# Kernel tuning notes

Measured on AMD Instinct MI355X. Metric: run time of the kernel, lower is better.

## Reference

```python
import jax, jax.numpy as jnp
import numpy as np

T, B, D, A, L = 256, 256, 512, 32, 3
EPS = 1e-6

def _layernorm(x, scale, bias):
    mu = jnp.mean(x, axis=-1, keepdims=True)
    var = jnp.mean(jnp.square(x - mu), axis=-1, keepdims=True)
    return (x - mu) * jax.lax.rsqrt(var + EPS) * scale + bias

def setup_inputs() -> dict:
    key = jax.random.key(0)
    ks = jax.random.split(key, 16)
    def orth(k, shape, scale):
        a = jax.random.normal(k, shape, dtype=jnp.float32)
        q, r = jnp.linalg.qr(a)
        q = q * jnp.sign(jnp.diagonal(r))
        return (scale * q).astype(jnp.float32)
    inp = {
        'hidden': jnp.zeros((B, D), jnp.float32),
        'obs': jax.random.normal(ks[0], (T, B, D), jnp.float32),
        'dones': jax.random.randint(ks[1], (T, B), 0, 2) > 0,
        'avail_actions': jax.random.randint(ks[2], (T, B, A), 0, 2).astype(jnp.int32),
        # MLP stack: 3 Dense(D) + LayerNorm
        'Wm': jnp.stack([orth(jax.random.fold_in(ks[3], l), (D, D), np.sqrt(2)) for l in range(L)]),
        'bm': jnp.zeros((L, D), jnp.float32),
        'lns': jnp.ones((L, D), jnp.float32),
        'lnb': jnp.zeros((L, D), jnp.float32),
        # GRUCell params: input denses ir/iz/in (with bias), hidden denses hr/hz (no bias), hn (bias)
        'Wi': jnp.stack([jax.random.normal(jax.random.fold_in(ks[4], g), (D, D), jnp.float32) / np.sqrt(D) for g in range(3)]),
        'bi': jnp.zeros((3, D), jnp.float32),
        'Wh': jnp.stack([orth(jax.random.fold_in(ks[5], g), (D, D), 1.0) for g in range(3)]),
        'bhn': jnp.zeros((D,), jnp.float32),
        # actor head
        'Wo': orth(ks[6], (D, D), 2.0),
        'bo': jnp.zeros((D,), jnp.float32),
        'ln2s': jnp.ones((D,), jnp.float32),
        'ln2b': jnp.zeros((D,), jnp.float32),
        'Wa': orth(ks[7], (D, A), 0.01),
        'ba': jnp.zeros((A,), jnp.float32),
    }
    return inp

def reference(hidden, obs, dones, avail_actions, Wm, bm, lns, lnb, Wi, bi, Wh, bhn, Wo, bo, ln2s, ln2b, Wa, ba):
    # MLP encoder: Dense -> LayerNorm -> ReLU, x num_layers
    e = obs  # [T,B,D]
    for l in range(Wm.shape[0]):
        e = jax.nn.relu(_layernorm(e @ Wm[l] + bm[l], lns[l], lnb[l]))
    # time-scanned GRU with reset-masked carry (reset -> zeros carry)
    def step(h, xs):
        x, d = xs  # x:[B,D], d:[B]
        h = jnp.where(d[:, None], jnp.zeros_like(h), h)
        r = jax.nn.sigmoid(x @ Wi[0] + bi[0] + h @ Wh[0])
        z = jax.nn.sigmoid(x @ Wi[1] + bi[1] + h @ Wh[1])
        n = jnp.tanh(x @ Wi[2] + bi[2] + r * (h @ Wh[2] + bhn))
        h_new = (1.0 - z) * n + z * h
        return h_new, h_new
    hidden, y = jax.lax.scan(step, hidden, (e, dones))  # y:[T,B,D]
    # actor head
    am = jax.nn.relu(_layernorm(y @ Wo + bo, ln2s, ln2b))
    logits = am @ Wa + ba
    unavail = 1.0 - avail_actions.astype(logits.dtype)
    action_logits = logits - unavail * 1e10
    return hidden, action_logits
```

## Files before the change

### kernel.cpp

```cpp
#include <hip/hip_runtime.h>
#include <hip/hip_bf16.h>
#include <math.h>


#define TTT 256
#define BBB 256
#define DDD 512
#define ACT 32
#define MMM (TTT*BBB)

typedef short bf16x8 __attribute__((ext_vector_type(8)));
typedef float f32x4 __attribute__((ext_vector_type(4)));
typedef unsigned short u16;

__device__ inline u16 f2bf(float f) {
    unsigned int u = __float_as_uint(f);
    u += 0x7fffu + ((u >> 16) & 1u);
    return (u16)(u >> 16);
}
__device__ inline float bf2f(u16 h) { return __uint_as_float(((unsigned int)h) << 16); }

__global__ __launch_bounds__(256) void transpose_cvt_k(
    const float* __restrict__ in, u16* __restrict__ out, int ostride)
{
    __shared__ float tile[32][33];
    const int c = threadIdx.x & 31;
    const int r0 = threadIdx.x >> 5;
    const int bx = blockIdx.x, by = blockIdx.y;
#pragma unroll
    for (int p = 0; p < 4; p++) {
        int r = r0 + p * 8;
        tile[r][c] = in[(size_t)(by * 32 + r) * DDD + bx * 32 + c];
    }
    __syncthreads();
#pragma unroll
    for (int p = 0; p < 4; p++) {
        int r = r0 + p * 8;
        out[(size_t)(bx * 32 + r) * ostride + by * 32 + c] = f2bf(tile[c][r]);
    }
}

template<bool AF32>
__global__ __launch_bounds__(256) void gemm_bf16_k(
    const void* __restrict__ Aptr, const u16* __restrict__ Bt,
    const float* __restrict__ bias, u16* __restrict__ C, int N)
{
    __shared__ u16 As[128 * 64];
    __shared__ u16 Bs[128 * 64];
    const int tid = threadIdx.x;
    const int row0 = blockIdx.x * 128;
    const int col0 = blockIdx.y * 128;
    const int lane = tid & 63, wid = tid >> 6;
    const int wr = wid >> 1, wc = wid & 1;
    const int lm = lane & 15, lq = lane >> 4;

    f32x4 acc[4][4];
#pragma unroll
    for (int i = 0; i < 4; i++)
#pragma unroll
        for (int j = 0; j < 4; j++) acc[i][j] = (f32x4){0.f, 0.f, 0.f, 0.f};

    for (int kc = 0; kc < 8; kc++) {
        const int k0 = kc * 64;
#pragma unroll
        for (int p = 0; p < 4; p++) {
            int g = p * 256 + tid;
            int row = g >> 3, j = g & 7;
            bf16x8 v;
            if (AF32) {
                const float* s = (const float*)Aptr + (size_t)(row0 + row) * DDD + k0 + j * 8;
                float4 a0 = *(const float4*)s;
                float4 a1 = *(const float4*)(s + 4);
                v[0] = (short)f2bf(a0.x); v[1] = (short)f2bf(a0.y);
                v[2] = (short)f2bf(a0.z); v[3] = (short)f2bf(a0.w);
                v[4] = (short)f2bf(a1.x); v[5] = (short)f2bf(a1.y);
                v[6] = (short)f2bf(a1.z); v[7] = (short)f2bf(a1.w);
            } else {
                v = *(const bf16x8*)((const u16*)Aptr + (size_t)(row0 + row) * DDD + k0 + j * 8);
            }
            *(bf16x8*)(As + row * 64 + ((j ^ (row & 7)) << 3)) = v;
        }
#pragma unroll
        for (int p = 0; p < 4; p++) {
            int g = p * 256 + tid;
            int n = g >> 3, j = g & 7;
            bf16x8 v = *(const bf16x8*)(Bt + (size_t)(col0 + n) * DDD + k0 + j * 8);
            *(bf16x8*)(Bs + n * 64 + ((j ^ (n & 7)) << 3)) = v;
        }
        __syncthreads();
#pragma unroll
        for (int ks = 0; ks < 2; ks++) {
            bf16x8 af[4], bfr[4];
#pragma unroll
            for (int i = 0; i < 4; i++) {
                int row = wr * 64 + i * 16 + lm;
                af[i] = *(const bf16x8*)(As + row * 64 + (((ks * 4 + lq) ^ (row & 7)) << 3));
            }
#pragma unroll
            for (int j = 0; j < 4; j++) {
                int n = wc * 64 + j * 16 + lm;
                bfr[j] = *(const bf16x8*)(Bs + n * 64 + (((ks * 4 + lq) ^ (n & 7)) << 3));
            }
#pragma unroll
            for (int i = 0; i < 4; i++)
#pragma unroll
                for (int j = 0; j < 4; j++)
                    acc[i][j] = __builtin_amdgcn_mfma_f32_16x16x32_bf16(af[i], bfr[j], acc[i][j], 0, 0, 0);
        }
        __syncthreads();
    }
#pragma unroll
    for (int j = 0; j < 4; j++) {
        int col = col0 + wc * 64 + j * 16 + lm;
        float bj = bias[col];
#pragma unroll
        for (int i = 0; i < 4; i++) {
            int rb = row0 + wr * 64 + i * 16 + lq * 4;
#pragma unroll
            for (int r = 0; r < 4; r++)
                C[(size_t)(rb + r) * N + col] = f2bf(acc[i][j][r] + bj);
        }
    }
}

__global__ __launch_bounds__(256) void ln_relu_k(
    u16* __restrict__ X, const float* __restrict__ gamma, const float* __restrict__ beta)
{
    const int tid = threadIdx.x;
    const int lane = tid & 63;
    const size_t row = (size_t)blockIdx.x * 4 + (tid >> 6);
    const int c0 = lane * 8;
    u16* px = X + row * DDD + c0;
    bf16x8 v = *(const bf16x8*)px;
    float f[8]; float s = 0.f, s2 = 0.f;
#pragma unroll
    for (int i = 0; i < 8; i++) { f[i] = bf2f((u16)v[i]); s += f[i]; s2 += f[i] * f[i]; }
#pragma unroll
    for (int off = 32; off; off >>= 1) { s += __shfl_xor(s, off); s2 += __shfl_xor(s2, off); }
    float mu = s * (1.f / (float)DDD);
    float rs = rsqrtf(s2 * (1.f / (float)DDD) - mu * mu + 1e-6f);
    float4 g0 = *(const float4*)(gamma + c0), g1 = *(const float4*)(gamma + c0 + 4);
    float4 b0 = *(const float4*)(beta + c0),  b1 = *(const float4*)(beta + c0 + 4);
    float gg[8] = {g0.x, g0.y, g0.z, g0.w, g1.x, g1.y, g1.z, g1.w};
    float bb[8] = {b0.x, b0.y, b0.z, b0.w, b1.x, b1.y, b1.z, b1.w};
    bf16x8 o;
#pragma unroll
    for (int i = 0; i < 8; i++) {
        float yv = (f[i] - mu) * rs * gg[i] + bb[i];
        o[i] = (short)f2bf(fmaxf(yv, 0.f));
    }
    *(bf16x8*)px = o;
}

__global__ __launch_bounds__(256) void logits_k(
    const u16* __restrict__ AM, const float* __restrict__ Wa,
    const float* __restrict__ ba, const int* __restrict__ avail,
    float* __restrict__ out)
{
    __shared__ float xs[8][DDD];
    const int tid = threadIdx.x;
    const size_t row0 = (size_t)blockIdx.x * 8;
    for (int g = tid; g < 8 * 64; g += 256) {
        int r = g >> 6, c8 = (g & 63) * 8;
        bf16x8 v = *(const bf16x8*)(AM + (row0 + r) * DDD + c8);
#pragma unroll
        for (int i = 0; i < 8; i++) xs[r][c8 + i] = bf2f((u16)v[i]);
    }
    __syncthreads();
    const int r = tid >> 5, a = tid & 31;
    float acc = 0.f;
    for (int k = 0; k < DDD; k += 4) {
        float4 xv = *(const float4*)&xs[r][k];
        acc = fmaf(xv.x, Wa[(k + 0) * ACT + a], acc);
        acc = fmaf(xv.y, Wa[(k + 1) * ACT + a], acc);
        acc = fmaf(xv.z, Wa[(k + 2) * ACT + a], acc);
        acc = fmaf(xv.w, Wa[(k + 3) * ACT + a], acc);
    }
    size_t o = (row0 + r) * ACT + a;
    float v = acc + ba[a];
    if (avail[o] == 0) v -= 1e10f;
    out[o] = v;
}

__global__ __launch_bounds__(256) void depth_build_k(
    const int* __restrict__ dones,
    int* __restrict__ keyA, int* __restrict__ pidxA,
    int* __restrict__ counts, int* __restrict__ maxk)
{
    __shared__ int lc[512];
    __shared__ int lmax;
    const int b = threadIdx.x;
    lc[b] = 0; lc[b + 256] = 0;
    if (b == 0) lmax = 0;
    __syncthreads();
    int dprev = 0, mx = 0;
    for (int t = 0; t < TTT; t++) {
        int pos = t * BBB + b;
        int d, pi, k;
        if (dones[pos] != 0)       { d = 0; pi = -1;       k = 0; }
        else if (t == 0)           { d = 0; pi = -2 - b;   k = 1; }
        else                       { d = dprev + 1; pi = pos - BBB; k = d + 1; }
        keyA[pos] = k; pidxA[pos] = pi;
        atomicAdd(&lc[k], 1);
        mx = max(mx, k);
        dprev = d;
    }
    atomicMax(&lmax, mx);
    __syncthreads();
    counts[b] = lc[b];
    counts[b + 256] = lc[b + 256];
    if (b == 0) *maxk = lmax;
}

__global__ void scan_k(const int* __restrict__ counts, int* __restrict__ offs)
{
    if (threadIdx.x == 0) {
        int s = 0;
        for (int i = 0; i < 512; i++) { offs[i] = s; s += counts[i]; }
    }
}

__global__ __launch_bounds__(256) void scatter_k(
    const int* __restrict__ keyA, const int* __restrict__ offs,
    int* __restrict__ cursor, int* __restrict__ list)
{
    __shared__ int lcnt[512];
    __shared__ int lbase[512];
    const int tid = threadIdx.x;
    lcnt[tid] = 0; lcnt[tid + 256] = 0;
    __syncthreads();
    int pos = blockIdx.x * 256 + tid;
    int k = keyA[pos];
    int rank = atomicAdd(&lcnt[k], 1);
    __syncthreads();
    for (int q = tid; q < 512; q += 256) {
        int c = lcnt[q];
        lbase[q] = c ? atomicAdd(&cursor[q], c) : 0;
    }
    __syncthreads();
    list[offs[k] + lbase[k] + rank] = pos;
}

__device__ inline void grid_barrier(int* cnt, int* gen, int nblk)
{
    __syncthreads();
    if (threadIdx.x == 0) {
        __threadfence();
        int g = __hip_atomic_load(gen, __ATOMIC_RELAXED, __HIP_MEMORY_SCOPE_AGENT);
        int a = __hip_atomic_fetch_add(cnt, 1, __ATOMIC_ACQ_REL, __HIP_MEMORY_SCOPE_AGENT);
        if (a == nblk - 1) {
            __hip_atomic_store(cnt, 0, __ATOMIC_RELAXED, __HIP_MEMORY_SCOPE_AGENT);
            __hip_atomic_store(gen, g + 1, __ATOMIC_RELEASE, __HIP_MEMORY_SCOPE_AGENT);
        } else {
            while (__hip_atomic_load(gen, __ATOMIC_RELAXED, __HIP_MEMORY_SCOPE_AGENT) == g)
                __builtin_amdgcn_s_sleep(4);
            (void)__hip_atomic_load(gen, __ATOMIC_ACQUIRE, __HIP_MEMORY_SCOPE_AGENT);
        }
        __threadfence();
    }
    __syncthreads();
}

template<bool YF32>
__global__ __launch_bounds__(256, 2) void gru_depth_k(
    const u16* __restrict__ E, const float* __restrict__ hidden,
    const u16* __restrict__ Wstk, const float* __restrict__ bi,
    const float* __restrict__ bhn,
    const int* __restrict__ list, const int* __restrict__ offs,
    const int* __restrict__ counts, const int* __restrict__ maxk,
    const int* __restrict__ pidxA,
    void* __restrict__ Yv, float* __restrict__ hid_out,
    int* __restrict__ barCnt, int* __restrict__ barGen)
{
    __shared__ u16 As[64 * 256];
    __shared__ int posL[64], pidxL[64];
    __shared__ int sAnyH;
    const int tid = threadIdx.x;
    const int w = tid >> 6, lane = tid & 63;
    const int lm = lane & 15, lq = lane >> 4;
    const int nblk = gridDim.x;
    const int e   = blockIdx.x & 7;
    const int xb  = blockIdx.x >> 3;
    const int nxb = nblk >> 3;

    const int MK = *maxk;
    for (int k = 0; k <= MK; k++) {
        const int nd = counts[k];
        const int off = offs[k];
        const int ntiles = (nd + 63) >> 6;
        const int ntl = (ntiles - e + 7) >> 3;
        const int njl = (ntl > 0) ? (ntl << 2) : 0;
        for (int lj = xb; lj < njl; lj += nxb) {
            const int rt = ((lj >> 2) << 3) + e;
            const int panel = lj & 3;
            bool hasH = false;
            if (tid < 64) {
                int idx = rt * 64 + tid;
                int p = (idx < nd) ? list[off + idx] : -1;
                int pi = (p >= 0) ? pidxA[p] : -1;
                posL[tid] = p;
                pidxL[tid] = pi;
                hasH = (p >= 0) && (pi != -1);
                unsigned long long m = __ballot(hasH);
                if (tid == 0) sAnyH = (m != 0ULL);
            }
            __syncthreads();
            const bool skipH = !sAnyH;

            f32x4 a01[4][4], aX[4][2], aH[4][2];
#pragma unroll
            for (int mt = 0; mt < 4; mt++) {
#pragma unroll
                for (int q = 0; q < 4; q++) a01[mt][q] = (f32x4){0.f, 0.f, 0.f, 0.f};
#pragma unroll
                for (int q = 0; q < 2; q++) {
                    aX[mt][q] = (f32x4){0.f, 0.f, 0.f, 0.f};
                    aH[mt][q] = (f32x4){0.f, 0.f, 0.f, 0.f};
                }
            }

            const int cb = panel * 128 + w * 32;
            const u16* wp[6];
#pragma unroll
            for (int ct = 0; ct < 6; ct++) {
                int gate = ct >> 1;
                int nglob = gate * 512 + cb + ((ct & 1) << 4) + lm;
                wp[ct] = Wstk + (size_t)nglob * 1024 + lq * 8;
            }

            const int nkc = skipH ? 2 : 4;
            for (int kc = 0; kc < nkc; kc++) {
#pragma unroll
                for (int it = 0; it < 8; it++) {
                    int g = it * 256 + tid;
                    int row = g >> 5, jg = g & 31;
                    int kglob = kc * 256 + jg * 8;
                    bf16x8 v = (bf16x8){0, 0, 0, 0, 0, 0, 0, 0};
                    int p = posL[row];
                    if (p >= 0) {
                        if (kglob < 512) {
                            v = *(const bf16x8*)(E + (size_t)p * DDD + kglob);
                        } else {
                            int k2 = kglob - 512;
                            int pi = pidxL[row];
                            if (pi >= 0) {
                                if (YF32) {
                                    const float* s = (const float*)Yv + (size_t)pi * DDD + k2;
                                    float4 a0 = *(const float4*)s;
                                    float4 a1 = *(const float4*)(s + 4);
                                    v[0] = (short)f2bf(a0.x); v[1] = (short)f2bf(a0.y);
                                    v[2] = (short)f2bf(a0.z); v[3] = (short)f2bf(a0.w);
                                    v[4] = (short)f2bf(a1.x); v[5] = (short)f2bf(a1.y);
                                    v[6] = (short)f2bf(a1.z); v[7] = (short)f2bf(a1.w);
                                } else {
                                    v = *(const bf16x8*)((const u16*)Yv + (size_t)pi * DDD + k2);
                                }
                            } else if (pi <= -2) {
                                const float* s = hidden + (size_t)(-pi - 2) * DDD + k2;
                                float4 a0 = *(const float4*)s;
                                float4 a1 = *(const float4*)(s + 4);
                                v[0] = (short)f2bf(a0.x); v[1] = (short)f2bf(a0.y);
                                v[2] = (short)f2bf(a0.z); v[3] = (short)f2bf(a0.w);
                                v[4] = (short)f2bf(a1.x); v[5] = (short)f2bf(a1.y);
                                v[6] = (short)f2bf(a1.z); v[7] = (short)f2bf(a1.w);
                            }
                        }
                    }
                    *(bf16x8*)(As + row * 256 + ((jg ^ (row & 31)) << 3)) = v;
                }
                __syncthreads();

                const bool xpart = (kc < 2);
                const int kgb = kc * 256;
                bf16x8 bfA[6], bfB[6];

#define LOADW(B, KG) \
    _Pragma("unroll") \
    for (int ct = 0; ct < 6; ct++) B[ct] = *(const bf16x8*)(wp[ct] + (KG));

#define COMPW(B, S) \
    _Pragma("unroll") \
    for (int mt = 0; mt < 4; mt++) { \
        int row = mt * 16 + lm; \
        int jgr = (S) * 4 + lq; \
        bf16x8 af = *(const bf16x8*)(As + row * 256 + ((jgr ^ (row & 31)) << 3)); \
        a01[mt][0] = __builtin_amdgcn_mfma_f32_16x16x32_bf16(af, B[0], a01[mt][0], 0, 0, 0); \
        a01[mt][1] = __builtin_amdgcn_mfma_f32_16x16x32_bf16(af, B[1], a01[mt][1], 0, 0, 0); \
        a01[mt][2] = __builtin_amdgcn_mfma_f32_16x16x32_bf16(af, B[2], a01[mt][2], 0, 0, 0); \
        a01[mt][3] = __builtin_amdgcn_mfma_f32_16x16x32_bf16(af, B[3], a01[mt][3], 0, 0, 0); \
        if (xpart) { \
            aX[mt][0] = __builtin_amdgcn_mfma_f32_16x16x32_bf16(af, B[4], aX[mt][0], 0, 0, 0); \
            aX[mt][1] = __builtin_amdgcn_mfma_f32_16x16x32_bf16(af, B[5], aX[mt][1], 0, 0, 0); \
        } else { \
            aH[mt][0] = __builtin_amdgcn_mfma_f32_16x16x32_bf16(af, B[4], aH[mt][0], 0, 0, 0); \
            aH[mt][1] = __builtin_amdgcn_mfma_f32_16x16x32_bf16(af, B[5], aH[mt][1], 0, 0, 0); \
        } \
    }

                LOADW(bfA, kgb + 0 * 32);
#pragma unroll
                for (int sp = 0; sp < 4; sp++) {
                    const int s0 = sp * 2, s1 = sp * 2 + 1;
                    LOADW(bfB, kgb + s1 * 32);
                    COMPW(bfA, s0);
                    if (sp < 3) { LOADW(bfA, kgb + (s1 + 1) * 32); }
                    COMPW(bfB, s1);
                }
#undef LOADW
#undef COMPW
                __syncthreads();
            }

#pragma unroll
            for (int mt = 0; mt < 4; mt++) {
#pragma unroll
                for (int r = 0; r < 4; r++) {
                    int row = mt * 16 + lq * 4 + r;
                    int p = posL[row];
                    if (p < 0) continue;
                    int pi = pidxL[row];
#pragma unroll
                    for (int ct = 0; ct < 2; ct++) {
                        int cglob = cb + ct * 16 + lm;
                        float rpre = a01[mt][ct][r]     + bi[cglob];
                        float zpre = a01[mt][2 + ct][r] + bi[512 + cglob];
                        float xn   = aX[mt][ct][r]      + bi[1024 + cglob];
                        float hn   = aH[mt][ct][r]      + bhn[cglob];
                        float rg = 1.f / (1.f + __expf(-rpre));
                        float zg = 1.f / (1.f + __expf(-zpre));
                        float targ = xn + rg * hn;
                        float t2 = __expf(-2.f * fabsf(targ));
                        float ng = copysignf((1.f - t2) / (1.f + t2), targ);
                        float hp = 0.f;
                        if (pi >= 0)
                            hp = YF32 ? ((const float*)Yv)[(size_t)pi * DDD + cglob]
                                      : bf2f(((const u16*)Yv)[(size_t)pi * DDD + cglob]);
                        else if (pi <= -2)
                            hp = hidden[(size_t)(-pi - 2) * DDD + cglob];
                        float hnew = (1.f - zg) * ng + zg * hp;
                        if (YF32) ((float*)Yv)[(size_t)p * DDD + cglob] = hnew;
                        else      ((u16*)Yv)[(size_t)p * DDD + cglob] = f2bf(hnew);
                    }
                }
            }
            __syncthreads();
        }
        grid_barrier(barCnt, barGen, nblk);
    }

    for (int i = blockIdx.x * 256 + tid; i < BBB * DDD; i += nblk * 256) {
        int b = i >> 9, c = i & 511;
        size_t yi = (size_t)(65280 + b) * DDD + c;
        hid_out[i] = YF32 ? ((const float*)Yv)[yi] : bf2f(((const u16*)Yv)[yi]);
    }
}

extern "C" void kernel_launch(void* const* d_in, const int* in_sizes, int n_in,
                              void* d_out, int out_size, void* d_ws, size_t ws_size,
                              hipStream_t stream)
{
    const float* hidden = (const float*)d_in[0];
    const float* obs    = (const float*)d_in[1];
    const int*   dones  = (const int*)d_in[2];
    const int*   avail  = (const int*)d_in[3];
    const float* Wm     = (const float*)d_in[4];
    const float* bm     = (const float*)d_in[5];
    const float* lns    = (const float*)d_in[6];
    const float* lnb    = (const float*)d_in[7];
    const float* Wi     = (const float*)d_in[8];
    const float* bi     = (const float*)d_in[9];
    const float* Wh     = (const float*)d_in[10];
    const float* bhn    = (const float*)d_in[11];
    const float* Wo     = (const float*)d_in[12];
    const float* bo     = (const float*)d_in[13];
    const float* ln2s   = (const float*)d_in[14];
    const float* ln2b   = (const float*)d_in[15];
    const float* Wa     = (const float*)d_in[16];
    const float* ba     = (const float*)d_in[17];
    float* out = (float*)d_out;

    char* w = (char*)d_ws;
    u16* Wstk = (u16*)w;  w += (size_t)1536 * 1024 * 2;
    u16* WmT  = (u16*)w;  w += (size_t)3 * DDD * DDD * 2;
    u16* WoT  = (u16*)w;  w += (size_t)DDD * DDD * 2;
    int* meta = (int*)w;  w += 8192;
    int* counts = meta;
    int* offs   = meta + 512;
    int* cursor = meta + 1024;
    int* maxk   = meta + 1536;
    int* barCnt = meta + 1568;
    int* barGen = meta + 1600;
    int* keyA   = (int*)w;  w += (size_t)MMM * 4;
    int* pidxA  = (int*)w;  w += (size_t)MMM * 4;
    int* list   = (int*)w;  w += (size_t)MMM * 4;
    u16* P = (u16*)w;       w += (size_t)MMM * DDD * 2;
    void* Yv = (void*)w;
    const size_t base = (size_t)(w - (char*)d_ws);
    const bool yf32 = (ws_size >= base + (size_t)MMM * DDD * 4);

    dim3 tgrid(16, 16);
    for (int l = 0; l < 3; l++)
        transpose_cvt_k<<<tgrid, 256, 0, stream>>>(Wm + (size_t)l * DDD * DDD, WmT + (size_t)l * DDD * DDD, DDD);
    transpose_cvt_k<<<tgrid, 256, 0, stream>>>(Wo, WoT, DDD);
    for (int g = 0; g < 3; g++) {
        transpose_cvt_k<<<tgrid, 256, 0, stream>>>(Wi + (size_t)g * DDD * DDD, Wstk + (size_t)g * 512 * 1024, 1024);
        transpose_cvt_k<<<tgrid, 256, 0, stream>>>(Wh + (size_t)g * DDD * DDD, Wstk + (size_t)g * 512 * 1024 + 512, 1024);
    }
    hipMemsetAsync(meta, 0, 8192, stream);

    depth_build_k<<<1, 256, 0, stream>>>(dones, keyA, pidxA, counts, maxk);
    scan_k<<<1, 64, 0, stream>>>(counts, offs);
    scatter_k<<<MMM / 256, 256, 0, stream>>>(keyA, offs, cursor, list);

    u16* Yq = (u16*)Yv;
    gemm_bf16_k<true><<<dim3(MMM / 128, 4), 256, 0, stream>>>(obs, WmT, bm, P, DDD);
    ln_relu_k<<<dim3(MMM / 4), 256, 0, stream>>>(P, lns, lnb);
    gemm_bf16_k<false><<<dim3(MMM / 128, 4), 256, 0, stream>>>(P, WmT + (size_t)DDD * DDD, bm + DDD, Yq, DDD);
    ln_relu_k<<<dim3(MMM / 4), 256, 0, stream>>>(Yq, lns + DDD, lnb + DDD);
    gemm_bf16_k<false><<<dim3(MMM / 128, 4), 256, 0, stream>>>(Yq, WmT + (size_t)2 * DDD * DDD, bm + 2 * DDD, P, DDD);
    ln_relu_k<<<dim3(MMM / 4), 256, 0, stream>>>(P, lns + 2 * DDD, lnb + 2 * DDD);

    {
        const void* fptr = yf32 ? (const void*)gru_depth_k<true>
                                : (const void*)gru_depth_k<false>;
        int occ = 0;
        hipError_t e = hipOccupancyMaxActiveBlocksPerMultiprocessor(&occ, fptr, 256, 0);
        if (e != hipSuccess || occ < 1) occ = 2;
        if (occ > 4) occ = 4;
        dim3 grid(occ * 256);
        if (yf32)
            gru_depth_k<true><<<grid, 256, 0, stream>>>(
                P, hidden, Wstk, bi, bhn, list, offs, counts, maxk, pidxA,
                Yv, out, barCnt, barGen);
        else
            gru_depth_k<false><<<grid, 256, 0, stream>>>(
                P, hidden, Wstk, bi, bhn, list, offs, counts, maxk, pidxA,
                Yv, out, barCnt, barGen);
    }

    if (yf32)
        gemm_bf16_k<true><<<dim3(MMM / 128, 4), 256, 0, stream>>>(Yv, WoT, bo, P, DDD);
    else
        gemm_bf16_k<false><<<dim3(MMM / 128, 4), 256, 0, stream>>>(Yv, WoT, bo, P, DDD);
    ln_relu_k<<<dim3(MMM / 4), 256, 0, stream>>>(P, ln2s, ln2b);
    logits_k<<<dim3(MMM / 8), 256, 0, stream>>>(P, Wa, ba, avail, out + BBB * DDD);
}
```

Measured before the change: 2.181 ms.

## Partition GRU depth scheduling per XCD and replace grid barrier with per-XCD counters

Splits the batch into 8 groups of 32 sequences, one per XCD (blockIdx & 7), building separate depth histograms, offsets and work lists for each group. Each group of blocks then advances through its own depth levels and synchronises only with blocks on the same XCD through a monotonic per-group counter, instead of a global generation barrier across all blocks. This removes cross-XCD barrier traffic and lets groups with shallower reset depth finish early. The cost is possible load imbalance between groups, and correctness relies on the blocks sharing an index modulo 8 seeing each other's writes at agent scope.

```diff
diff --git a/kernel.cpp b/kernel.cpp
--- a/kernel.cpp
+++ b/kernel.cpp
@@ -19,6 +19,8 @@
     return (u16)(u >> 16);
 }
 __device__ inline float bf2f(u16 h) { return __uint_as_float(((unsigned int)h) << 16); }
+
+#define AL_RLX(p)  __hip_atomic_load((p), __ATOMIC_RELAXED, __HIP_MEMORY_SCOPE_AGENT)
 
 __global__ __launch_bounds__(256) void transpose_cvt_k(
     const float* __restrict__ in, u16* __restrict__ out, int ostride)
@@ -187,11 +189,12 @@
     int* __restrict__ keyA, int* __restrict__ pidxA,
     int* __restrict__ counts, int* __restrict__ maxk)
 {
-    __shared__ int lc[512];
-    __shared__ int lmax;
+    __shared__ int lc[8 * 512];
+    __shared__ int lmax[8];
     const int b = threadIdx.x;
-    lc[b] = 0; lc[b + 256] = 0;
-    if (b == 0) lmax = 0;
+    const int e = b >> 5;
+    for (int i = b; i < 8 * 512; i += 256) lc[i] = 0;
+    if (b < 8) lmax[b] = 0;
     __syncthreads();
     int dprev = 0, mx = 0;
     for (int t = 0; t < TTT; t++) {
@@ -201,22 +204,22 @@
         else if (t == 0)           { d = 0; pi = -2 - b;   k = 1; }
         else                       { d = dprev + 1; pi = pos - BBB; k = d + 1; }
         keyA[pos] = k; pidxA[pos] = pi;
-        atomicAdd(&lc[k], 1);
+        atomicAdd(&lc[e * 512 + k], 1);
         mx = max(mx, k);
         dprev = d;
     }
-    atomicMax(&lmax, mx);
-    __syncthreads();
-    counts[b] = lc[b];
-    counts[b + 256] = lc[b + 256];
-    if (b == 0) *maxk = lmax;
+    atomicMax(&lmax[e], mx);
+    __syncthreads();
+    for (int i = b; i < 8 * 512; i += 256) counts[i] = lc[i];
+    if (b < 8) maxk[b] = lmax[b];
 }
 
 __global__ void scan_k(const int* __restrict__ counts, int* __restrict__ offs)
 {
-    if (threadIdx.x == 0) {
+    int e = threadIdx.x;
+    if (e < 8) {
         int s = 0;
-        for (int i = 0; i < 512; i++) { offs[i] = s; s += counts[i]; }
+        for (int i = 0; i < 512; i++) { offs[e * 512 + i] = s; s += counts[e * 512 + i]; }
     }
 }
 
@@ -224,155 +227,119 @@
     const int* __restrict__ keyA, const int* __restrict__ offs,
     int* __restrict__ cursor, int* __restrict__ list)
 {
-    __shared__ int lcnt[512];
-    __shared__ int lbase[512];
+    __shared__ int lcnt[8 * 512];
+    __shared__ int lbase[8 * 512];
     const int tid = threadIdx.x;
-    lcnt[tid] = 0; lcnt[tid + 256] = 0;
+    for (int i = tid; i < 8 * 512; i += 256) lcnt[i] = 0;
     __syncthreads();
     int pos = blockIdx.x * 256 + tid;
+    int b = pos & 255;
+    int e = b >> 5;
     int k = keyA[pos];
-    int rank = atomicAdd(&lcnt[k], 1);
-    __syncthreads();
-    for (int q = tid; q < 512; q += 256) {
+    int rank = atomicAdd(&lcnt[e * 512 + k], 1);
+    __syncthreads();
+    for (int q = tid; q < 8 * 512; q += 256) {
         int c = lcnt[q];
         lbase[q] = c ? atomicAdd(&cursor[q], c) : 0;
     }
     __syncthreads();
-    list[offs[k] + lbase[k] + rank] = pos;
-}
-
-__device__ inline void grid_barrier(int* cnt, int* gen, int nblk)
-{
-    __syncthreads();
-    if (threadIdx.x == 0) {
-        __threadfence();
-        int g = __hip_atomic_load(gen, __ATOMIC_RELAXED, __HIP_MEMORY_SCOPE_AGENT);
-        int a = __hip_atomic_fetch_add(cnt, 1, __ATOMIC_ACQ_REL, __HIP_MEMORY_SCOPE_AGENT);
-        if (a == nblk - 1) {
-            __hip_atomic_store(cnt, 0, __ATOMIC_RELAXED, __HIP_MEMORY_SCOPE_AGENT);
-            __hip_atomic_store(gen, g + 1, __ATOMIC_RELEASE, __HIP_MEMORY_SCOPE_AGENT);
-        } else {
-            while (__hip_atomic_load(gen, __ATOMIC_RELAXED, __HIP_MEMORY_SCOPE_AGENT) == g)
-                __builtin_amdgcn_s_sleep(4);
-            (void)__hip_atomic_load(gen, __ATOMIC_ACQUIRE, __HIP_MEMORY_SCOPE_AGENT);
-        }
-        __threadfence();
-    }
-    __syncthreads();
+    list[e * 8192 + offs[e * 512 + k] + lbase[e * 512 + k] + rank] = pos;
 }
 
 template<bool YF32>
-__global__ __launch_bounds__(256, 2) void gru_depth_k(
+__device__ __forceinline__ void gru_job(
     const u16* __restrict__ E, const float* __restrict__ hidden,
     const u16* __restrict__ Wstk, const float* __restrict__ bi,
     const float* __restrict__ bhn,
-    const int* __restrict__ list, const int* __restrict__ offs,
-    const int* __restrict__ counts, const int* __restrict__ maxk,
-    const int* __restrict__ pidxA,
-    void* __restrict__ Yv, float* __restrict__ hid_out,
-    int* __restrict__ barCnt, int* __restrict__ barGen)
-{
-    __shared__ u16 As[64 * 256];
-    __shared__ int posL[64], pidxL[64];
-    __shared__ int sAnyH;
+    const int* __restrict__ list, const int* __restrict__ pidxA,
+    void* __restrict__ Yv,
+    int off, int nd, int rt, int panel,
+    u16* As, int* posL, int* pidxL, int* sAnyH)
+{
     const int tid = threadIdx.x;
     const int w = tid >> 6, lane = tid & 63;
     const int lm = lane & 15, lq = lane >> 4;
-    const int nblk = gridDim.x;
-    const int e   = blockIdx.x & 7;
-    const int xb  = blockIdx.x >> 3;
-    const int nxb = nblk >> 3;
-
-    const int MK = *maxk;
-    for (int k = 0; k <= MK; k++) {
-        const int nd = counts[k];
-        const int off = offs[k];
-        const int ntiles = (nd + 63) >> 6;
-        const int ntl = (ntiles - e + 7) >> 3;
-        const int njl = (ntl > 0) ? (ntl << 2) : 0;
-        for (int lj = xb; lj < njl; lj += nxb) {
-            const int rt = ((lj >> 2) << 3) + e;
-            const int panel = lj & 3;
-            bool hasH = false;
-            if (tid < 64) {
-                int idx = rt * 64 + tid;
-                int p = (idx < nd) ? list[off + idx] : -1;
-                int pi = (p >= 0) ? pidxA[p] : -1;
-                posL[tid] = p;
-                pidxL[tid] = pi;
-                hasH = (p >= 0) && (pi != -1);
-                unsigned long long m = __ballot(hasH);
-                if (tid == 0) sAnyH = (m != 0ULL);
-            }
-            __syncthreads();
-            const bool skipH = !sAnyH;
-
-            f32x4 a01[4][4], aX[4][2], aH[4][2];
-#pragma unroll
-            for (int mt = 0; mt < 4; mt++) {
-#pragma unroll
-                for (int q = 0; q < 4; q++) a01[mt][q] = (f32x4){0.f, 0.f, 0.f, 0.f};
-#pragma unroll
-                for (int q = 0; q < 2; q++) {
-                    aX[mt][q] = (f32x4){0.f, 0.f, 0.f, 0.f};
-                    aH[mt][q] = (f32x4){0.f, 0.f, 0.f, 0.f};
+
+    bool hasH = false;
+    if (tid < 64) {
+        int idx = rt * 64 + tid;
+        int p = (idx < nd) ? list[off + idx] : -1;
+        int pi = (p >= 0) ? pidxA[p] : -1;
+        posL[tid] = p;
+        pidxL[tid] = pi;
+        hasH = (p >= 0) && (pi != -1);
+        unsigned long long m = __ballot(hasH);
+        if (tid == 0) *sAnyH = (m != 0ULL);
+    }
+    __syncthreads();
+    const bool skipH = !(*sAnyH);
+
+    f32x4 a01[4][4], aX[4][2], aH[4][2];
+#pragma unroll
+    for (int mt = 0; mt < 4; mt++) {
+#pragma unroll
+        for (int q = 0; q < 4; q++) a01[mt][q] = (f32x4){0.f, 0.f, 0.f, 0.f};
+#pragma unroll
+        for (int q = 0; q < 2; q++) {
+            aX[mt][q] = (f32x4){0.f, 0.f, 0.f, 0.f};
+            aH[mt][q] = (f32x4){0.f, 0.f, 0.f, 0.f};
+        }
+    }
+
+    const int cb = panel * 128 + w * 32;
+    const u16* wp[6];
+#pragma unroll
+    for (int ct = 0; ct < 6; ct++) {
+        int gate = ct >> 1;
+        int nglob = gate * 512 + cb + ((ct & 1) << 4) + lm;
+        wp[ct] = Wstk + (size_t)nglob * 1024 + lq * 8;
+    }
+
+    const int nkc = skipH ? 2 : 4;
+    for (int kc = 0; kc < nkc; kc++) {
+#pragma unroll
+        for (int it = 0; it < 8; it++) {
+            int g = it * 256 + tid;
+            int row = g >> 5, jg = g & 31;
+            int kglob = kc * 256 + jg * 8;
+            bf16x8 v = (bf16x8){0, 0, 0, 0, 0, 0, 0, 0};
+            int p = posL[row];
+            if (p >= 0) {
+                if (kglob < 512) {
+                    v = *(const bf16x8*)(E + (size_t)p * DDD + kglob);
+                } else {
+                    int k2 = kglob - 512;
+                    int pi = pidxL[row];
+                    if (pi >= 0) {
+                        if (YF32) {
+                            const float* s = (const float*)Yv + (size_t)pi * DDD + k2;
+                            float4 a0 = *(const float4*)s;
+                            float4 a1 = *(const float4*)(s + 4);
+                            v[0] = (short)f2bf(a0.x); v[1] = (short)f2bf(a0.y);
+                            v[2] = (short)f2bf(a0.z); v[3] = (short)f2bf(a0.w);
+                            v[4] = (short)f2bf(a1.x); v[5] = (short)f2bf(a1.y);
+                            v[6] = (short)f2bf(a1.z); v[7] = (short)f2bf(a1.w);
+                        } else {
+                            v = *(const bf16x8*)((const u16*)Yv + (size_t)pi * DDD + k2);
+                        }
+                    } else if (pi <= -2) {
+                        const float* s = hidden + (size_t)(-pi - 2) * DDD + k2;
+                        float4 a0 = *(const float4*)s;
+                        float4 a1 = *(const float4*)(s + 4);
+                        v[0] = (short)f2bf(a0.x); v[1] = (short)f2bf(a0.y);
+                        v[2] = (short)f2bf(a0.z); v[3] = (short)f2bf(a0.w);
+                        v[4] = (short)f2bf(a1.x); v[5] = (short)f2bf(a1.y);
+                        v[6] = (short)f2bf(a1.z); v[7] = (short)f2bf(a1.w);
+                    }
                 }
             }
-
-            const int cb = panel * 128 + w * 32;
-            const u16* wp[6];
-#pragma unroll
-            for (int ct = 0; ct < 6; ct++) {
-                int gate = ct >> 1;
-                int nglob = gate * 512 + cb + ((ct & 1) << 4) + lm;
-                wp[ct] = Wstk + (size_t)nglob * 1024 + lq * 8;
-            }
-
-            const int nkc = skipH ? 2 : 4;
-            for (int kc = 0; kc < nkc; kc++) {
-#pragma unroll
-                for (int it = 0; it < 8; it++) {
-                    int g = it * 256 + tid;
-                    int row = g >> 5, jg = g & 31;
-                    int kglob = kc * 256 + jg * 8;
-                    bf16x8 v = (bf16x8){0, 0, 0, 0, 0, 0, 0, 0};
-                    int p = posL[row];
-                    if (p >= 0) {
-                        if (kglob < 512) {
-                            v = *(const bf16x8*)(E + (size_t)p * DDD + kglob);
-                        } else {
-                            int k2 = kglob - 512;
-                            int pi = pidxL[row];
-                            if (pi >= 0) {
-                                if (YF32) {
-                                    const float* s = (const float*)Yv + (size_t)pi * DDD + k2;
-                                    float4 a0 = *(const float4*)s;
-                                    float4 a1 = *(const float4*)(s + 4);
-                                    v[0] = (short)f2bf(a0.x); v[1] = (short)f2bf(a0.y);
-                                    v[2] = (short)f2bf(a0.z); v[3] = (short)f2bf(a0.w);
-                                    v[4] = (short)f2bf(a1.x); v[5] = (short)f2bf(a1.y);
-                                    v[6] = (short)f2bf(a1.z); v[7] = (short)f2bf(a1.w);
-                                } else {
-                                    v = *(const bf16x8*)((const u16*)Yv + (size_t)pi * DDD + k2);
-                                }
-                            } else if (pi <= -2) {
-                                const float* s = hidden + (size_t)(-pi - 2) * DDD + k2;
-                                float4 a0 = *(const float4*)s;
-                                float4 a1 = *(const float4*)(s + 4);
-                                v[0] = (short)f2bf(a0.x); v[1] = (short)f2bf(a0.y);
-                                v[2] = (short)f2bf(a0.z); v[3] = (short)f2bf(a0.w);
-                                v[4] = (short)f2bf(a1.x); v[5] = (short)f2bf(a1.y);
-                                v[6] = (short)f2bf(a1.z); v[7] = (short)f2bf(a1.w);
-                            }
-                        }
-                    }
-                    *(bf16x8*)(As + row * 256 + ((jg ^ (row & 31)) << 3)) = v;
-                }
-                __syncthreads();
-
-                const bool xpart = (kc < 2);
-                const int kgb = kc * 256;
-                bf16x8 bfA[6], bfB[6];
+            *(bf16x8*)(As + row * 256 + ((jg ^ (row & 31)) << 3)) = v;
+        }
+        __syncthreads();
+
+        const bool xpart = (kc < 2);
+        const int kgb = kc * 256;
+        bf16x8 bfA[6], bfB[6];
 
 #define LOADW(B, KG) \
     _Pragma("unroll") \
@@ -397,61 +364,105 @@
         } \
     }
 
-                LOADW(bfA, kgb + 0 * 32);
-#pragma unroll
-                for (int sp = 0; sp < 4; sp++) {
-                    const int s0 = sp * 2, s1 = sp * 2 + 1;
-                    LOADW(bfB, kgb + s1 * 32);
-                    COMPW(bfA, s0);
-                    if (sp < 3) { LOADW(bfA, kgb + (s1 + 1) * 32); }
-                    COMPW(bfB, s1);
-                }
+        LOADW(bfA, kgb + 0 * 32);
+#pragma unroll
+        for (int sp = 0; sp < 4; sp++) {
+            const int s0 = sp * 2, s1 = sp * 2 + 1;
+            LOADW(bfB, kgb + s1 * 32);
+            COMPW(bfA, s0);
+            if (sp < 3) { LOADW(bfA, kgb + (s1 + 1) * 32); }
+            COMPW(bfB, s1);
+        }
 #undef LOADW
 #undef COMPW
-                __syncthreads();
+        __syncthreads();
+    }
+
+#pragma unroll
+    for (int mt = 0; mt < 4; mt++) {
+#pragma unroll
+        for (int r = 0; r < 4; r++) {
+            int row = mt * 16 + lq * 4 + r;
+            int p = posL[row];
+            if (p < 0) continue;
+            int pi = pidxL[row];
+#pragma unroll
+            for (int ct = 0; ct < 2; ct++) {
+                int cglob = cb + ct * 16 + lm;
+                float rpre = a01[mt][ct][r]     + bi[cglob];
+                float zpre = a01[mt][2 + ct][r] + bi[512 + cglob];
+                float xn   = aX[mt][ct][r]      + bi[1024 + cglob];
+                float hn   = aH[mt][ct][r]      + bhn[cglob];
+                float rg = 1.f / (1.f + __expf(-rpre));
+                float zg = 1.f / (1.f + __expf(-zpre));
+                float targ = xn + rg * hn;
+                float t2 = __expf(-2.f * fabsf(targ));
+                float ng = copysignf((1.f - t2) / (1.f + t2), targ);
+                float hp = 0.f;
+                if (pi >= 0)
+                    hp = YF32 ? ((const float*)Yv)[(size_t)pi * DDD + cglob]
+                              : bf2f(((const u16*)Yv)[(size_t)pi * DDD + cglob]);
+                else if (pi <= -2)
+                    hp = hidden[(size_t)(-pi - 2) * DDD + cglob];
+                float hnew = (1.f - zg) * ng + zg * hp;
+                if (YF32) ((float*)Yv)[(size_t)p * DDD + cglob] = hnew;
+                else      ((u16*)Yv)[(size_t)p * DDD + cglob] = f2bf(hnew);
             }
-
-#pragma unroll
-            for (int mt = 0; mt < 4; mt++) {
-#pragma unroll
-                for (int r = 0; r < 4; r++) {
-                    int row = mt * 16 + lq * 4 + r;
-                    int p = posL[row];
-                    if (p < 0) continue;
-                    int pi = pidxL[row];
-#pragma unroll
-                    for (int ct = 0; ct < 2; ct++) {
-                        int cglob = cb + ct * 16 + lm;
-                        float rpre = a01[mt][ct][r]     + bi[cglob];
-                        float zpre = a01[mt][2 + ct][r] + bi[512 + cglob];
-                        float xn   = aX[mt][ct][r]      + bi[1024 + cglob];
-                        float hn   = aH[mt][ct][r]      + bhn[cglob];
-                        float rg = 1.f / (1.f + __expf(-rpre));
-                        float zg = 1.f / (1.f + __expf(-zpre));
-                        float targ = xn + rg * hn;
-                        float t2 = __expf(-2.f * fabsf(targ));
-                        float ng = copysignf((1.f - t2) / (1.f + t2), targ);
-                        float hp = 0.f;
-                        if (pi >= 0)
-                            hp = YF32 ? ((const float*)Yv)[(size_t)pi * DDD + cglob]
-                                      : bf2f(((const u16*)Yv)[(size_t)pi * DDD + cglob]);
-                        else if (pi <= -2)
-                            hp = hidden[(size_t)(-pi - 2) * DDD + cglob];
-                        float hnew = (1.f - zg) * ng + zg * hp;
-                        if (YF32) ((float*)Yv)[(size_t)p * DDD + cglob] = hnew;
-                        else      ((u16*)Yv)[(size_t)p * DDD + cglob] = f2bf(hnew);
-                    }
-                }
-            }
-            __syncthreads();
-        }
-        grid_barrier(barCnt, barGen, nblk);
-    }
-
-    for (int i = blockIdx.x * 256 + tid; i < BBB * DDD; i += nblk * 256) {
-        int b = i >> 9, c = i & 511;
+        }
+    }
+    __syncthreads();
+}
+
+template<bool YF32>
+__global__ __launch_bounds__(256, 2) void gru_depth_k(
+    const u16* __restrict__ E, const float* __restrict__ hidden,
+    const u16* __restrict__ Wstk, const float* __restrict__ bi,
+    const float* __restrict__ bhn,
+    const int* __restrict__ list, const int* __restrict__ offs,
+    const int* __restrict__ counts, const int* __restrict__ maxk,
+    const int* __restrict__ pidxA,
+    void* __restrict__ Yv, float* __restrict__ hid_out,
+    int* __restrict__ xcdCnt)
+{
+    __shared__ u16 As[64 * 256];
+    __shared__ int posL[64], pidxL[64];
+    __shared__ int sAnyH;
+    const int tid = threadIdx.x;
+    const int nblk = gridDim.x;
+    const int e   = blockIdx.x & 7;
+    const int xb  = blockIdx.x >> 3;
+    const int nxb = nblk >> 3;
+
+    const int MKe = maxk[e];
+    const int* cnt_e = counts + e * 512;
+    const int* off_e = offs + e * 512;
+    const int lb = e * 8192;
+    int* cnt = xcdCnt + e * 32;
+    int round = 0;
+
+    for (int k = 0; k <= MKe; k++) {
+        const int nd = cnt_e[k];
+        const int off = lb + off_e[k];
+        const int njobs = ((nd + 63) >> 6) << 2;
+        for (int lj = xb; lj < njobs; lj += nxb) {
+            gru_job<YF32>(E, hidden, Wstk, bi, bhn, list, pidxA, Yv,
+                          off, nd, lj >> 2, lj & 3, As, posL, pidxL, &sAnyH);
+        }
+        ++round;
+        __syncthreads();
+        if (tid == 0) {
+            __hip_atomic_fetch_add(cnt, 1, __ATOMIC_RELAXED, __HIP_MEMORY_SCOPE_AGENT);
+            const int target = round * nxb;
+            while (AL_RLX(cnt) < target) __builtin_amdgcn_s_sleep(1);
+        }
+        __syncthreads();
+    }
+
+    for (int i = xb * 256 + tid; i < 32 * DDD; i += nxb * 256) {
+        int b = 32 * e + (i >> 9), c = i & 511;
         size_t yi = (size_t)(65280 + b) * DDD + c;
-        hid_out[i] = YF32 ? ((const float*)Yv)[yi] : bf2f(((const u16*)Yv)[yi]);
+        hid_out[(size_t)b * DDD + c] =
+            YF32 ? ((const float*)Yv)[yi] : bf2f(((const u16*)Yv)[yi]);
     }
 }
 
@@ -483,13 +494,12 @@
     u16* Wstk = (u16*)w;  w += (size_t)1536 * 1024 * 2;
     u16* WmT  = (u16*)w;  w += (size_t)3 * DDD * DDD * 2;
     u16* WoT  = (u16*)w;  w += (size_t)DDD * DDD * 2;
-    int* meta = (int*)w;  w += 8192;
+    int* meta = (int*)w;  w += 65536;
     int* counts = meta;
-    int* offs   = meta + 512;
-    int* cursor = meta + 1024;
-    int* maxk   = meta + 1536;
-    int* barCnt = meta + 1568;
-    int* barGen = meta + 1600;
+    int* offs   = meta + 4096;
+    int* cursor = meta + 8192;
+    int* maxk   = meta + 12288;
+    int* xcdCnt = meta + 12544;
     int* keyA   = (int*)w;  w += (size_t)MMM * 4;
     int* pidxA  = (int*)w;  w += (size_t)MMM * 4;
     int* list   = (int*)w;  w += (size_t)MMM * 4;
@@ -506,7 +516,7 @@
         transpose_cvt_k<<<tgrid, 256, 0, stream>>>(Wi + (size_t)g * DDD * DDD, Wstk + (size_t)g * 512 * 1024, 1024);
         transpose_cvt_k<<<tgrid, 256, 0, stream>>>(Wh + (size_t)g * DDD * DDD, Wstk + (size_t)g * 512 * 1024 + 512, 1024);
     }
-    hipMemsetAsync(meta, 0, 8192, stream);
+    hipMemsetAsync(meta, 0, 65536, stream);
 
     depth_build_k<<<1, 256, 0, stream>>>(dones, keyA, pidxA, counts, maxk);
     scan_k<<<1, 64, 0, stream>>>(counts, offs);
@@ -524,18 +534,18 @@
         const void* fptr = yf32 ? (const void*)gru_depth_k<true>
                                 : (const void*)gru_depth_k<false>;
         int occ = 0;
-        hipError_t e = hipOccupancyMaxActiveBlocksPerMultiprocessor(&occ, fptr, 256, 0);
-        if (e != hipSuccess || occ < 1) occ = 2;
+        hipError_t err = hipOccupancyMaxActiveBlocksPerMultiprocessor(&occ, fptr, 256, 0);
+        if (err != hipSuccess || occ < 1) occ = 2;
         if (occ > 4) occ = 4;
         dim3 grid(occ * 256);
         if (yf32)
             gru_depth_k<true><<<grid, 256, 0, stream>>>(
                 P, hidden, Wstk, bi, bhn, list, offs, counts, maxk, pidxA,
-                Yv, out, barCnt, barGen);
+                Yv, out, xcdCnt);
         else
             gru_depth_k<false><<<grid, 256, 0, stream>>>(
                 P, hidden, Wstk, bi, bhn, list, offs, counts, maxk, pidxA,
-                Yv, out, barCnt, barGen);
+                Yv, out, xcdCnt);
     }
 
     if (yf32)
```

Result: faster. 1.881 ms (-13.8%).
